# Optimization experiments

Measured on AMD Instinct MI355X. Metric: run time of the kernel, lower is better.

Reference implementation:

```python
import jax, jax.numpy as jnp
import numpy as np

L_ITERS = 8   # number of ReduNet layers
C = 10        # number of classes
D = 1024      # feature dimension
N = 4096      # number of samples (columns of Z)


def setup_inputs() -> dict:
    key = jax.random.key(0)
    k0, k1, k2, k3 = jax.random.split(key, 4)
    Z = jax.random.normal(k0, (D, N), dtype=jnp.float32)
    # column-normalized features, as the net maintains at every layer
    Z = Z / jnp.linalg.norm(Z, axis=0, keepdims=True)
    # Elist[l]: (D,D) expansion operator; Cslist[l]: (C,D,D) per-class compression operators
    Elist = jax.random.normal(k1, (L_ITERS, D, D), dtype=jnp.float32) / np.float32(np.sqrt(D))
    Cslist = jax.random.normal(k2, (L_ITERS, C, D, D), dtype=jnp.float32) / np.float32(np.sqrt(D))
    gamma = jax.random.uniform(k3, (C,), dtype=jnp.float32)
    gamma = gamma / jnp.sum(gamma)
    eta = jnp.asarray(0.5, dtype=jnp.float32)
    temperature = jnp.asarray(0.1, dtype=jnp.float32)
    return {"Z": Z, "Elist": Elist, "Cslist": Cslist, "gamma": gamma,
            "eta": eta, "temperature": temperature, "L": L_ITERS}


def reference(Z, Elist, Cslist, gamma, eta, temperature, L):
    for l in range(L):
        Cs = Cslist[l]                                   # (C, d, d)
        CZ = jnp.einsum('cij,jn->cin', Cs, Z)            # (C, d, n)
        sims = -jnp.sqrt(jnp.sum(CZ * CZ, axis=1))       # fro norm over dim=1 -> (C, n)
        P_hat = jax.nn.softmax(sims / temperature, axis=0)  # softmax over classes
        PZ = P_hat[:, None, :] * Z                       # (C, d, n)
        term = jnp.einsum('c,cij,cjn->in', gamma, Cs, PZ)   # gamma-weighted class compression
        grads = Elist[l] @ Z - term                      # (d, n)
        Z = Z + eta * grads
        Z = Z / jnp.linalg.norm(Z, axis=0, keepdims=True)   # column-wise normalization
    return Z
```

## Files before the change

kernel.cpp:

```cpp
#include <hip/hip_runtime.h>
#include <hip/hip_bf16.h>
#include <stdint.h>

#define D_DIM 1024
#define N_DIM 4096
#define C_CLS 10
#define L_IT 8
#define M_DIM 11264
#define NBM 44

typedef __bf16 bf16_t;
typedef __bf16 bf16x8 __attribute__((ext_vector_type(8)));
typedef __bf16 bf16x4 __attribute__((ext_vector_type(4)));
typedef float  f32x4  __attribute__((ext_vector_type(4)));
typedef unsigned short u16x8 __attribute__((ext_vector_type(8)));

__device__ __forceinline__ float bf2f(uint16_t u) {
  union { uint32_t i; float f; } x; x.i = ((uint32_t)u) << 16; return x.f;
}

__global__ __launch_bounds__(256) void pack_w(const float4* __restrict__ Cs,
                                              const float4* __restrict__ El,
                                              bf16x4* __restrict__ dst) {
  const int CS4 = C_CLS * D_DIM * D_DIM / 4;
  int i = blockIdx.x * 256 + threadIdx.x;
  float4 v = (i < CS4) ? Cs[i] : El[i - CS4];
  bf16x4 o;
  o[0] = (bf16_t)v.x; o[1] = (bf16_t)v.y; o[2] = (bf16_t)v.z; o[3] = (bf16_t)v.w;
  dst[i] = o;
}

__global__ __launch_bounds__(256) void init_zt(const float* __restrict__ Zin,
                                               float* __restrict__ ZfT,
                                               bf16_t* __restrict__ ZbT) {
  __shared__ float tile[32][33];
  int tx = threadIdx.x & 31, ty = threadIdx.x >> 5;
  int nb = blockIdx.x, db = blockIdx.y;
  int n = nb * 32 + tx;
#pragma unroll
  for (int j = 0; j < 32; j += 8) {
    int d = db * 32 + ty + j;
    tile[ty + j][tx] = Zin[(size_t)d * N_DIM + n];
  }
  __syncthreads();
  int d2 = db * 32 + tx;
#pragma unroll
  for (int j = 0; j < 32; j += 8) {
    int n2 = nb * 32 + ty + j;
    float v = tile[tx][ty + j];
    ZfT[(size_t)n2 * D_DIM + d2] = v;
    ZbT[(size_t)n2 * D_DIM + d2] = (bf16_t)v;
  }
}

__global__ __launch_bounds__(256) void final_out(const float* __restrict__ ZfT,
                                                 float* __restrict__ outp) {
  __shared__ float tile[32][33];
  int tx = threadIdx.x & 31, ty = threadIdx.x >> 5;
  int nb = blockIdx.x, db = blockIdx.y;
#pragma unroll
  for (int j = 0; j < 32; j += 8) {
    int n = nb * 32 + ty + j;
    int d = db * 32 + tx;
    tile[ty + j][tx] = ZfT[(size_t)n * D_DIM + d];
  }
  __syncthreads();
#pragma unroll
  for (int j = 0; j < 32; j += 8) {
    int d2 = db * 32 + ty + j;
    int n2 = nb * 32 + tx;
    outp[(size_t)d2 * N_DIM + n2] = tile[tx][ty + j];
  }
}


#define SA(buf, h, t) do {                                                              \
    _Pragma("unroll") for (int e_ = 0; e_ < 2; ++e_) {                                  \
      const bf16_t* s_ = Wb + aoff0[e_] + (size_t)(h) * 65536 + (size_t)(t) * 64;       \
      __builtin_amdgcn_global_load_lds(                                                 \
        (const __attribute__((address_space(1))) void*)s_,                              \
        (__attribute__((address_space(3))) void*)(lds + (buf)*16384 + (h)*8192 + dstslot[e_]), \
        16, 0, 0);                                                                      \
    } } while (0)

#define SBst(buf, h, t) do {                                                            \
    _Pragma("unroll") for (int e_ = 0; e_ < 2; ++e_) {                                  \
      const bf16_t* s_ = ZbT + boff0[e_] + (size_t)(h) * 32768 + (size_t)(t) * 64;      \
      __builtin_amdgcn_global_load_lds(                                                 \
        (const __attribute__((address_space(1))) void*)s_,                              \
        (__attribute__((address_space(3))) void*)(lds + 32768 + (buf)*16384 + (h)*8192 + dstslot[e_]), \
        16, 0, 0);                                                                      \
    } } while (0)

#define LOAD_A(buf, qm) do {                                                            \
    _Pragma("unroll") for (int f_ = 0; f_ < 4; ++f_)                                    \
      _Pragma("unroll") for (int kk_ = 0; kk_ < 2; ++kk_)                               \
        a[f_][kk_] = *(const bf16x8*)(lds + (buf)*16384 + (qm)*8192 + aRowBase + f_*1024 + sidx[kk_]); \
  } while (0)

#define LOAD_Bq(buf, qn, arr) do {                                                      \
    _Pragma("unroll") for (int f_ = 0; f_ < 2; ++f_)                                    \
      _Pragma("unroll") for (int kk_ = 0; kk_ < 2; ++kk_)                               \
        arr[f_][kk_] = *(const bf16x8*)(lds + 32768 + (buf)*16384 + (qn)*8192 + bRowBase + f_*1024 + sidx[kk_]); \
  } while (0)

#define MFMAQ(qm, qn, arr) do {                                                         \
    _Pragma("unroll") for (int mm_ = 0; mm_ < 4; ++mm_)                                 \
      _Pragma("unroll") for (int nn_ = 0; nn_ < 2; ++nn_)                               \
        _Pragma("unroll") for (int kk_ = 0; kk_ < 2; ++kk_)                             \
          acc[(qm)*4+mm_][(qn)*2+nn_] = __builtin_amdgcn_mfma_f32_16x16x32_bf16(        \
            a[mm_][kk_], arr[nn_][kk_], acc[(qm)*4+mm_][(qn)*2+nn_], 0, 0, 0);          \
  } while (0)

#define BAR   __builtin_amdgcn_s_barrier()
#define VM(n) asm volatile("s_waitcnt vmcnt(" #n ")" ::: "memory")
#define LGKM8 asm volatile("s_waitcnt lgkmcnt(8)" ::: "memory")
#define PRIO1 __builtin_amdgcn_s_setprio(1)
#define PRIO0 __builtin_amdgcn_s_setprio(0)

#define PH8(qm, qn, arr, LOADS, STAGES, PREBAR, POSTMFMA) do {                          \
    LOADS;                                                                              \
    STAGES;                                                                             \
    PREBAR;                                                                             \
    BAR;                                                                                \
    asm volatile("s_waitcnt lgkmcnt(0)" ::: "memory");                                  \
    PRIO1;                                                                              \
    MFMAQ(qm, qn, arr);                                                                 \
    PRIO0;                                                                              \
    POSTMFMA;                                                                           \
    BAR;                                                                                \
  } while (0)

__global__ __launch_bounds__(512, 2) void gemm_wz8(const bf16_t* __restrict__ Wb,
                                                   const bf16_t* __restrict__ ZbT,
                                                   bf16_t* __restrict__ OUT_T, int ldn,
                                                   float* __restrict__ ssq) {
  __shared__ __align__(16) bf16_t lds[65536];

  int nwg = gridDim.x;
  int bid = blockIdx.x;
  int q = nwg >> 3, r = nwg & 7;
  int xcd = bid & 7, idx = bid >> 3;
  int swz = (xcd < r ? xcd * (q + 1) : r * (q + 1) + (xcd - r) * q) + idx;
  int bm = swz >> 4, bn = swz & 15;
  int m0 = bm * 256, n0 = bn * 256;

  int tid = threadIdx.x;
  int wave = tid >> 6, lane = tid & 63;
  int wrow = wave >> 2, wcol = wave & 3;
  int lm = lane & 15, lks = lane >> 4;
  int sw = lm & 7;

  size_t aoff0[2], boff0[2];
  int dstslot[2];
#pragma unroll
  for (int e = 0; e < 2; ++e) {
    int j = e * 512 + tid;
    int rih = j >> 3, sl = j & 7;
    int sg = sl ^ (rih & 7);
    int arow = (rih & 63) + ((rih >> 6) << 7);
    int brow = (rih & 31) + ((rih >> 5) << 6);
    aoff0[e] = (size_t)(m0 + arow) * 1024 + sg * 8;
    boff0[e] = (size_t)(n0 + brow) * 1024 + sg * 8;
    dstslot[e] = e * 4096 + wave * 512;
  }

  int aRowBase = (wrow * 64 + lm) * 64;
  int bRowBase = (wcol * 32 + lm) * 64;
  int sidx[2] = { ((0 + lks) ^ sw) * 8, ((4 + lks) ^ sw) * 8 };

  f32x4 acc[8][4] = {};
  bf16x8 a[4][2], b0[2][2], b1[2][2];

  SA(0, 0, 0); SBst(0, 0, 0); SBst(0, 1, 0); SA(0, 1, 0);
  SA(1, 0, 1); SBst(1, 0, 1); SBst(1, 1, 1);
  VM(6);
  BAR;

  for (int it = 0; it < 8; ++it) {
    int tO = 2 * it + 1, tN = 2 * it + 2, tM = 2 * it + 3;
    bool st = (it < 7);

    PH8(0, 0, b0, LOAD_A(0, 0); LOAD_Bq(0, 0, b0), SA(1, 1, tO), LGKM8, );
    PH8(0, 1, b1, LOAD_Bq(0, 1, b1), { if (st) SA(0, 0, tN); }, , );
    PH8(1, 0, b0, LOAD_A(0, 1), { if (st) SBst(0, 0, tN); }, , );
    PH8(1, 1, b1, , { if (st) SBst(0, 1, tN); }, ,
        { if (st) { VM(6); } else { VM(0); } });
    PH8(0, 0, b0, LOAD_A(1, 0); LOAD_Bq(1, 0, b0), { if (st) SA(0, 1, tN); }, LGKM8, );
    PH8(0, 1, b1, LOAD_Bq(1, 1, b1), { if (st) SA(1, 0, tM); }, , );
    PH8(1, 0, b0, LOAD_A(1, 1), { if (st) SBst(1, 0, tM); }, , );
    PH8(1, 1, b1, , { if (st) SBst(1, 1, tM); }, , { if (st) VM(6); });
  }

#pragma unroll
  for (int mf = 0; mf < 8; ++mf)
#pragma unroll
    for (int nf = 0; nf < 4; ++nf) {
      int col = n0 + wcol * 64 + nf * 16 + lm;
      int row = m0 + wrow * 128 + mf * 16 + lks * 4;
      bf16x4 v;
#pragma unroll
      for (int rr = 0; rr < 4; ++rr) v[rr] = (bf16_t)acc[mf][nf][rr];
      *(bf16x4*)(OUT_T + (size_t)col * M_DIM + row) = v;
    }

  if (m0 < C_CLS * 1024) {
    int c = m0 >> 10;
#pragma unroll
    for (int nf = 0; nf < 4; ++nf) {
      float v = 0.f;
#pragma unroll
      for (int mf = 0; mf < 8; ++mf)
#pragma unroll
        for (int rr = 0; rr < 4; ++rr)
          v += acc[mf][nf][rr] * acc[mf][nf][rr];
      v += __shfl_xor(v, 16);
      v += __shfl_xor(v, 32);
      if (lks == 0)
        atomicAdd(&ssq[(size_t)c * ldn + n0 + wcol * 64 + nf * 16 + lm], v);
    }
  }
}

__global__ __launch_bounds__(256) void update2(const bf16_t* __restrict__ OUT_T, int Nc,
                                               const float* __restrict__ ssq,
                                               const float* __restrict__ gamma,
                                               const float* __restrict__ etap,
                                               const float* __restrict__ tempr,
                                               float* __restrict__ ZfT,
                                               bf16_t* __restrict__ ZbT,
                                               int n_off) {
  int wv = threadIdx.x >> 6, lane = threadIdx.x & 63;
  int nl = blockIdx.x * 4 + wv;
  if (nl >= Nc) return;
  int n = n_off + nl;
  float eta = etap[0], invT = 1.0f / tempr[0];

  float s[C_CLS], m = -1e30f;
#pragma unroll
  for (int c = 0; c < C_CLS; ++c) {
    float sim = -sqrtf(ssq[(size_t)c * Nc + nl]);
    s[c] = sim;
    m = fmaxf(m, sim);
  }
  float sum = 0.f;
#pragma unroll
  for (int c = 0; c < C_CLS; ++c) {
    float e = __expf((s[c] - m) * invT);
    s[c] = e;
    sum += e;
  }
  float invsum = 1.0f / sum;
  float gP[C_CLS];
#pragma unroll
  for (int c = 0; c < C_CLS; ++c) gP[c] = gamma[c] * s[c] * invsum;

  const u16x8* ob = (const u16x8*)(OUT_T + (size_t)nl * M_DIM) + lane * 2;
  float term[16] = {};
#pragma unroll
  for (int c = 0; c < C_CLS; ++c) {
    u16x8 v0 = ob[c * 128], v1 = ob[c * 128 + 1];
#pragma unroll
    for (int j = 0; j < 8; ++j) {
      term[j]     += gP[c] * bf2f(v0[j]);
      term[8 + j] += gP[c] * bf2f(v1[j]);
    }
  }
  u16x8 g0 = ob[C_CLS * 128], g1 = ob[C_CLS * 128 + 1];

  const f32x4* zp = (const f32x4*)(ZfT + (size_t)n * D_DIM) + lane * 4;
  f32x4 z[4] = { zp[0], zp[1], zp[2], zp[3] };

  float zn[16];
  float ss = 0.f;
#pragma unroll
  for (int j = 0; j < 16; ++j) {
    float g = bf2f(j < 8 ? g0[j & 7] : g1[j & 7]);
    float v = z[j >> 2][j & 3] + eta * (g - term[j]);
    zn[j] = v;
    ss += v * v;
  }
#pragma unroll
  for (int k = 1; k < 64; k <<= 1) ss += __shfl_xor(ss, k);
  float inv = rsqrtf(ss);

  f32x4* zo = (f32x4*)(ZfT + (size_t)n * D_DIM) + lane * 4;
  bf16x8* bo = (bf16x8*)(ZbT + (size_t)n * D_DIM) + lane * 2;
#pragma unroll
  for (int q4 = 0; q4 < 4; ++q4) {
    f32x4 o;
#pragma unroll
    for (int j = 0; j < 4; ++j) o[j] = zn[q4 * 4 + j] * inv;
    zo[q4] = o;
  }
#pragma unroll
  for (int h = 0; h < 2; ++h) {
    bf16x8 o;
#pragma unroll
    for (int j = 0; j < 8; ++j) o[j] = (bf16_t)(zn[h * 8 + j] * inv);
    bo[h] = o;
  }
}

extern "C" void kernel_launch(void* const* d_in, const int* in_sizes, int n_in,
                              void* d_out, int out_size, void* d_ws, size_t ws_size,
                              hipStream_t stream) {
  (void)in_sizes; (void)n_in; (void)out_size;
  const float* Zin        = (const float*)d_in[0];
  const float* Elist      = (const float*)d_in[1];
  const float* Cslist     = (const float*)d_in[2];
  const float* gamma      = (const float*)d_in[3];
  const float* eta        = (const float*)d_in[4];
  const float* temperature= (const float*)d_in[5];

  auto align256 = [](size_t x) { return (x + 255) & ~(size_t)255; };
  size_t zbt_b = align256((size_t)N_DIM * D_DIM * 2);
  size_t zft_b = align256((size_t)N_DIM * D_DIM * 4);
  size_t wb_b  = align256((size_t)M_DIM * D_DIM * 2);
  size_t ssq_b = align256((size_t)L_IT * C_CLS * N_DIM * 4);
  size_t out_b = align256((size_t)M_DIM * N_DIM * 2);

  if (zbt_b + zft_b + wb_b + ssq_b + out_b > ws_size) {
    hipMemsetAsync(d_out, 0, (size_t)D_DIM * N_DIM * 4, stream);
    return;
  }

  char* p = (char*)d_ws;
  bf16_t* ZbT  = (bf16_t*)p; p += zbt_b;
  float*  ZfT  = (float*)p;  p += zft_b;
  bf16_t* Wb   = (bf16_t*)p; p += wb_b;
  float*  ssq  = (float*)p;  p += ssq_b;
  bf16_t* OUT_T= (bf16_t*)p;

  hipMemsetAsync(ssq, 0, (size_t)L_IT * C_CLS * N_DIM * 4, stream);
  init_zt<<<dim3(N_DIM / 32, D_DIM / 32), 256, 0, stream>>>(Zin, ZfT, ZbT);

  for (int l = 0; l < L_IT; ++l) {
    const float* Cs = Cslist + (size_t)l * C_CLS * D_DIM * D_DIM;
    const float* El = Elist  + (size_t)l * D_DIM * D_DIM;
    float* ssq_l = ssq + (size_t)l * C_CLS * N_DIM;

    pack_w<<<dim3(M_DIM * D_DIM / 4 / 256), 256, 0, stream>>>(
        (const float4*)Cs, (const float4*)El, (bf16x4*)Wb);

    gemm_wz8<<<dim3(NBM * (N_DIM / 256)), 512, 0, stream>>>(
        Wb, ZbT, OUT_T, N_DIM, ssq_l);
    update2<<<dim3(N_DIM / 4), 256, 0, stream>>>(
        OUT_T, N_DIM, ssq_l, gamma, eta, temperature, ZfT, ZbT, 0);
  }
  final_out<<<dim3(N_DIM / 32, D_DIM / 32), 256, 0, stream>>>(ZfT, (float*)d_out);
}
```

Measured before the change: 1.221 ms.

## Fuse next-layer weight packing into update kernel with double-buffered weights

Removes the separate per-layer pack_w launch. The fp32-to-bf16 conversion of the next layer's weights now runs as extra blocks inside the update kernel, and the first layer's packing is merged into the init transpose kernel. Two weight buffers alternate between layers so packing layer l+1 does not overwrite the weights layer l is still using. This saves kernel launches and lets the memory-bound packing overlap with the small update work, at the cost of an extra 22 MB workspace buffer.

New measurement: 1.201 ms. Within noise of the previous version (-1.7%).

```diff
diff --git a/kernel.cpp b/kernel.cpp
--- a/kernel.cpp
+++ b/kernel.cpp
@@ -8,6 +8,8 @@
 #define L_IT 8
 #define M_DIM 11264
 #define NBM 44
+#define PACK_BLOCKS 11264
+#define UPD_BLOCKS 1024
 
 typedef __bf16 bf16_t;
 typedef __bf16 bf16x8 __attribute__((ext_vector_type(8)));
@@ -19,23 +21,30 @@
   union { uint32_t i; float f; } x; x.i = ((uint32_t)u) << 16; return x.f;
 }
 
-__global__ __launch_bounds__(256) void pack_w(const float4* __restrict__ Cs,
-                                              const float4* __restrict__ El,
-                                              bf16x4* __restrict__ dst) {
+__device__ __forceinline__ void pack_body(const float4* __restrict__ Cs,
+                                          const float4* __restrict__ El,
+                                          bf16x4* __restrict__ dst, int i) {
   const int CS4 = C_CLS * D_DIM * D_DIM / 4;
-  int i = blockIdx.x * 256 + threadIdx.x;
   float4 v = (i < CS4) ? Cs[i] : El[i - CS4];
   bf16x4 o;
   o[0] = (bf16_t)v.x; o[1] = (bf16_t)v.y; o[2] = (bf16_t)v.z; o[3] = (bf16_t)v.w;
   dst[i] = o;
 }
 
-__global__ __launch_bounds__(256) void init_zt(const float* __restrict__ Zin,
-                                               float* __restrict__ ZfT,
-                                               bf16_t* __restrict__ ZbT) {
+__global__ __launch_bounds__(256) void init_pack(const float* __restrict__ Zin,
+                                                 float* __restrict__ ZfT,
+                                                 bf16_t* __restrict__ ZbT,
+                                                 const float4* __restrict__ Cs0,
+                                                 const float4* __restrict__ El0,
+                                                 bf16x4* __restrict__ Wb0) {
+  if (blockIdx.x < PACK_BLOCKS) {
+    pack_body(Cs0, El0, Wb0, blockIdx.x * 256 + threadIdx.x);
+    return;
+  }
+  int idx = blockIdx.x - PACK_BLOCKS;
+  int nb = idx & 127, db = idx >> 7;
   __shared__ float tile[32][33];
   int tx = threadIdx.x & 31, ty = threadIdx.x >> 5;
-  int nb = blockIdx.x, db = blockIdx.y;
   int n = nb * 32 + tx;
 #pragma unroll
   for (int j = 0; j < 32; j += 8) {
@@ -222,18 +231,23 @@
   }
 }
 
-__global__ __launch_bounds__(256) void update2(const bf16_t* __restrict__ OUT_T, int Nc,
-                                               const float* __restrict__ ssq,
-                                               const float* __restrict__ gamma,
-                                               const float* __restrict__ etap,
-                                               const float* __restrict__ tempr,
-                                               float* __restrict__ ZfT,
-                                               bf16_t* __restrict__ ZbT,
-                                               int n_off) {
+__global__ __launch_bounds__(256) void update_pack(const bf16_t* __restrict__ OUT_T, int Nc,
+                                                   const float* __restrict__ ssq,
+                                                   const float* __restrict__ gamma,
+                                                   const float* __restrict__ etap,
+                                                   const float* __restrict__ tempr,
+                                                   float* __restrict__ ZfT,
+                                                   bf16_t* __restrict__ ZbT,
+                                                   const float4* __restrict__ CsN,
+                                                   const float4* __restrict__ ElN,
+                                                   bf16x4* __restrict__ WbN) {
+  if (blockIdx.x >= UPD_BLOCKS) {
+    pack_body(CsN, ElN, WbN, (blockIdx.x - UPD_BLOCKS) * 256 + threadIdx.x);
+    return;
+  }
   int wv = threadIdx.x >> 6, lane = threadIdx.x & 63;
   int nl = blockIdx.x * 4 + wv;
-  if (nl >= Nc) return;
-  int n = n_off + nl;
+  int n = nl;
   float eta = etap[0], invT = 1.0f / tempr[0];
 
   float s[C_CLS], m = -1e30f;
@@ -320,7 +334,7 @@
   size_t ssq_b = align256((size_t)L_IT * C_CLS * N_DIM * 4);
   size_t out_b = align256((size_t)M_DIM * N_DIM * 2);
 
-  if (zbt_b + zft_b + wb_b + ssq_b + out_b > ws_size) {
+  if (zbt_b + zft_b + 2 * wb_b + ssq_b + out_b > ws_size) {
     hipMemsetAsync(d_out, 0, (size_t)D_DIM * N_DIM * 4, stream);
     return;
   }
@@ -328,25 +342,36 @@
   char* p = (char*)d_ws;
   bf16_t* ZbT  = (bf16_t*)p; p += zbt_b;
   float*  ZfT  = (float*)p;  p += zft_b;
-  bf16_t* Wb   = (bf16_t*)p; p += wb_b;
+  bf16_t* Wb0  = (bf16_t*)p; p += wb_b;
+  bf16_t* Wb1  = (bf16_t*)p; p += wb_b;
   float*  ssq  = (float*)p;  p += ssq_b;
   bf16_t* OUT_T= (bf16_t*)p;
+  bf16_t* Wbs[2] = { Wb0, Wb1 };
 
   hipMemsetAsync(ssq, 0, (size_t)L_IT * C_CLS * N_DIM * 4, stream);
-  init_zt<<<dim3(N_DIM / 32, D_DIM / 32), 256, 0, stream>>>(Zin, ZfT, ZbT);
+
+  init_pack<<<dim3(PACK_BLOCKS + 4096), 256, 0, stream>>>(
+      Zin, ZfT, ZbT,
+      (const float4*)Cslist, (const float4*)Elist, (bf16x4*)Wb0);
 
   for (int l = 0; l < L_IT; ++l) {
-    const float* Cs = Cslist + (size_t)l * C_CLS * D_DIM * D_DIM;
-    const float* El = Elist  + (size_t)l * D_DIM * D_DIM;
     float* ssq_l = ssq + (size_t)l * C_CLS * N_DIM;
-
-    pack_w<<<dim3(M_DIM * D_DIM / 4 / 256), 256, 0, stream>>>(
-        (const float4*)Cs, (const float4*)El, (bf16x4*)Wb);
+    bf16_t* Wb = Wbs[l & 1];
 
     gemm_wz8<<<dim3(NBM * (N_DIM / 256)), 512, 0, stream>>>(
         Wb, ZbT, OUT_T, N_DIM, ssq_l);
-    update2<<<dim3(N_DIM / 4), 256, 0, stream>>>(
-        OUT_T, N_DIM, ssq_l, gamma, eta, temperature, ZfT, ZbT, 0);
+
+    if (l + 1 < L_IT) {
+      const float* CsN = Cslist + (size_t)(l + 1) * C_CLS * D_DIM * D_DIM;
+      const float* ElN = Elist  + (size_t)(l + 1) * D_DIM * D_DIM;
+      update_pack<<<dim3(UPD_BLOCKS + PACK_BLOCKS), 256, 0, stream>>>(
+          OUT_T, N_DIM, ssq_l, gamma, eta, temperature, ZfT, ZbT,
+          (const float4*)CsN, (const float4*)ElN, (bf16x4*)Wbs[(l + 1) & 1]);
+    } else {
+      update_pack<<<dim3(UPD_BLOCKS), 256, 0, stream>>>(
+          OUT_T, N_DIM, ssq_l, gamma, eta, temperature, ZfT, ZbT,
+          nullptr, nullptr, nullptr);
+    }
   }
   final_out<<<dim3(N_DIM / 32, D_DIM / 32), 256, 0, stream>>>(ZfT, (float*)d_out);
 }
```
